# Kernel tuning notes

Measured on AMD Instinct MI355X. Metric: run time of the kernel, lower is better.

The kernel has to match this reference:

```python
import jax, jax.numpy as jnp
import numpy as np

BN_EPS = 1e-5

def _conv1x1(x, w, b):
    # x: [B,C,H,W], w: [O,C], b: [O] -> [B,O,H,W]
    return jnp.einsum('bchw,oc->bohw', x, w) + b[None, :, None, None]

def setup_inputs() -> dict:
    key = jax.random.key(0)
    ks = jax.random.split(key, 9)
    B, C, H, W = 8, 256, 64, 64
    I = C // 2
    s_in = 1.0 / np.sqrt(C)
    s_out = 1.0 / np.sqrt(I)
    return {
        'x':       jax.random.normal(ks[0], (B, C, H, W), dtype=jnp.float32),
        'g_w':     jax.random.uniform(ks[1], (I, C), jnp.float32, -s_in, s_in),
        'g_b':     jax.random.uniform(ks[2], (I,),  jnp.float32, -s_in, s_in),
        'theta_w': jax.random.uniform(ks[3], (I, C), jnp.float32, -s_in, s_in),
        'theta_b': jax.random.uniform(ks[4], (I,),  jnp.float32, -s_in, s_in),
        'phi_w':   jax.random.uniform(ks[5], (I, C), jnp.float32, -s_in, s_in),
        'phi_b':   jax.random.uniform(ks[6], (I,),  jnp.float32, -s_in, s_in),
        'w_w':     jax.random.uniform(ks[7], (C, I), jnp.float32, -s_out, s_out),
        'w_b':     jax.random.uniform(ks[8], (C,),  jnp.float32, -s_out, s_out),
        'gamma':   jnp.ones((C,), dtype=jnp.float32),   # BN weight init constant 1
        'beta':    jnp.zeros((C,), dtype=jnp.float32),  # BN bias init constant 0
    }

def reference(x, g_w, g_b, theta_w, theta_b, phi_w, phi_b, w_w, w_b, gamma, beta):
    B, C, H, W = x.shape
    I = g_w.shape[0]
    N = H * W
    g_x     = _conv1x1(x, g_w, g_b).reshape(B, I, N)          # [B,I,N]
    theta_x = _conv1x1(x, theta_w, theta_b).reshape(B, I, N)  # [B,I,N]
    phi_x   = _conv1x1(x, phi_w, phi_b).reshape(B, I, N)      # [B,I,N]
    # f = theta^T @ phi : [B,N,N]
    f = jnp.einsum('bin,bim->bnm', theta_x, phi_x)
    a = jax.nn.softmax(f, axis=-1)
    # y = a @ g^T : [B,N,I] -> [B,I,H,W]
    y = jnp.einsum('bnm,bim->bin', a, g_x).reshape(B, I, H, W)
    wy = _conv1x1(y, w_w, w_b)                                # [B,C,H,W]
    # BatchNorm2d (training mode: batch statistics over B,H,W per channel)
    mean = jnp.mean(wy, axis=(0, 2, 3), keepdims=True)
    var = jnp.var(wy, axis=(0, 2, 3), keepdims=True)
    wy_bn = (wy - mean) * jax.lax.rsqrt(var + BN_EPS)
    wy_bn = wy_bn * gamma[None, :, None, None] + beta[None, :, None, None]
    return wy_bn + x
```

## Files before the change

kernel.cpp:

```cpp
#include <hip/hip_runtime.h>

#define B_ 8
#define C_ 256
#define I_ 128
#define N_ 4096
#define BN_ (B_ * N_)
#define LOG2E 1.4426950408889634f

typedef __attribute__((ext_vector_type(8))) short bf16x8;
typedef __attribute__((ext_vector_type(4))) float f32x4;
typedef __attribute__((ext_vector_type(4))) int i32x4;

static __device__ __forceinline__ short f2bf(float f) {
    unsigned u = __float_as_uint(f);
    unsigned r = u + 0x7fffu + ((u >> 16) & 1u);
    return (short)(r >> 16);
}
static __device__ __forceinline__ float bf2f(short s) {
    return __uint_as_float(((unsigned)(unsigned short)s) << 16);
}
static __device__ __forceinline__ unsigned cvt_pk_bf16(float lo, float hi) {
    unsigned r;
    asm("v_cvt_pk_bf16_f32 %0, %1, %2" : "=v"(r) : "v"(lo), "v"(hi));
    return r;
}

__global__ void k_prep(const float* g_w, const float* theta_w, const float* phi_w,
                       const float* g_b, const float* theta_b, const float* phi_b,
                       const float* w_w, short* wcat, short* wwb, float* bcat) {
    int i = blockIdx.x * 256 + threadIdx.x;
    if (i < 384 * 256) {
        int j = i >> 8, c = i & 255;
        float v = (j < 128) ? theta_w[j * 256 + c] * LOG2E
                : (j < 256) ? phi_w[(j - 128) * 256 + c]
                            : g_w[(j - 256) * 256 + c];
        wcat[i] = f2bf(v);
    } else if (i < 384 * 256 + 256 * 128) {
        int k = i - 384 * 256;
        wwb[k] = f2bf(w_w[k]);
    } else if (i < 384 * 256 + 256 * 128 + 384) {
        int j = i - (384 * 256 + 256 * 128);
        bcat[j] = (j < 128) ? theta_b[j] * LOG2E
                : (j < 256) ? phi_b[j - 128] : g_b[j - 256];
    }
}

__global__ __launch_bounds__(256) void k_proj(const float* __restrict__ x,
                                              const short* __restrict__ wcat,
                                              const float* __restrict__ bcat,
                                              short* __restrict__ tp,
                                              short* __restrict__ gmat) {
    int b = blockIdx.y;
    int n0 = blockIdx.x * 64;
    int tid = threadIdx.x;
    int wave = tid >> 6, lane = tid & 63, s = lane & 15, q = lane >> 4;
    __shared__ short xs[64][264];

#pragma unroll
    for (int it = 0; it < 16; ++it) {
        int cr = (tid >> 4) + it * 16;
        int nc = tid & 15;
        const float4 v = *(const float4*)&x[((size_t)b * C_ + cr) * N_ + n0 + nc * 4];
        xs[nc * 4 + 0][cr] = f2bf(v.x);
        xs[nc * 4 + 1][cr] = f2bf(v.y);
        xs[nc * 4 + 2][cr] = f2bf(v.z);
        xs[nc * 4 + 3][cr] = f2bf(v.w);
    }
    __syncthreads();

    f32x4 acc[4][6];
#pragma unroll
    for (int rt = 0; rt < 4; ++rt)
#pragma unroll
        for (int jt = 0; jt < 6; ++jt) acc[rt][jt] = (f32x4){0.f, 0.f, 0.f, 0.f};

#pragma unroll
    for (int kb = 0; kb < 8; ++kb) {
        bf16x8 af[4], bfv[6];
#pragma unroll
        for (int rt = 0; rt < 4; ++rt)
            af[rt] = *(const bf16x8*)&xs[rt * 16 + s][kb * 32 + q * 8];
#pragma unroll
        for (int jt = 0; jt < 6; ++jt)
            bfv[jt] = *(const bf16x8*)&wcat[(wave * 96 + jt * 16 + s) * 256 + kb * 32 + q * 8];
#pragma unroll
        for (int rt = 0; rt < 4; ++rt)
#pragma unroll
            for (int jt = 0; jt < 6; ++jt)
                acc[rt][jt] = __builtin_amdgcn_mfma_f32_16x16x32_bf16(af[rt], bfv[jt], acc[rt][jt], 0, 0, 0);
    }

#pragma unroll
    for (int rt = 0; rt < 4; ++rt)
#pragma unroll
        for (int jt = 0; jt < 6; ++jt) {
            int j = wave * 96 + jt * 16 + s;
            float bias = bcat[j];
#pragma unroll
            for (int r = 0; r < 4; ++r) {
                int n = n0 + rt * 16 + 4 * q + r;
                float v = acc[rt][jt][r] + bias;
                if (j < 256)
                    tp[((size_t)b * N_ + n) * 256 + j] = f2bf(v);
                else
                    gmat[((size_t)b * I_ + (j - 256)) * N_ + n] = f2bf(v);
            }
        }
}

__global__ __launch_bounds__(512, 2) void k_attn_wy(const short* __restrict__ tp,
                                                    const short* __restrict__ gmat,
                                                    const short* __restrict__ wwb,
                                                    const float* __restrict__ w_b,
                                                    short* __restrict__ wyh) {
    int id = blockIdx.x;
    int b = id & 7;
    int qt = id >> 3;
    int n0 = qt * 128;
    int tid = threadIdx.x;
    int wave = tid >> 6, lane = tid & 63, s = lane & 15, q = lane >> 4;
    int kg = wave >> 2, qg = wave & 3;

    __shared__ __align__(16) short SH[65536];
    __shared__ float l_lds[2][128];
    char* base = (char*)SH;

    const int swz = (s & 7) << 4;
    int kA[4];
#pragma unroll
    for (int kb = 0; kb < 4; ++kb) kA[kb] = s * 256 + ((kb * 64 + q * 16) ^ swz);
    int vA[2];
#pragma unroll
    for (int kb2 = 0; kb2 < 2; ++kb2) vA[kb2] = s * 256 + ((kb2 * 64 + q * 16) ^ swz);
    int krow = tid >> 4, kch = tid & 15;
    int stW = krow * 256 + ((kch * 16) ^ ((krow & 7) << 4));

    i32x4 onesw = (i32x4){0x3F803F80, 0x3F803F80, 0x3F803F80, 0x3F803F80};
    bf16x8 vone = __builtin_bit_cast(bf16x8, onesw);

    bf16x8 qf[2][4];
#pragma unroll
    for (int fr = 0; fr < 2; ++fr) {
        const short* qb = tp + ((size_t)b * N_ + n0 + qg * 32 + fr * 16 + s) * 256;
#pragma unroll
        for (int kb = 0; kb < 4; ++kb) qf[fr][kb] = *(const bf16x8*)(qb + kb * 32 + q * 8);
    }

    f32x4 ot[2][8];
#pragma unroll
    for (int fr = 0; fr < 2; ++fr)
#pragma unroll
        for (int t = 0; t < 8; ++t) ot[fr][t] = (f32x4){0.f, 0.f, 0.f, 0.f};
    f32x4 lacc[2] = {(f32x4){0.f, 0.f, 0.f, 0.f}, (f32x4){0.f, 0.f, 0.f, 0.f}};

    bf16x8 pk[4], pv[4];
#pragma unroll
    for (int it = 0; it < 4; ++it) {
        pk[it] = *(const bf16x8*)&tp[((size_t)b * N_ + krow + it * 32) * 256 + 128 + kch * 8];
        pv[it] = *(const bf16x8*)&gmat[((size_t)b * I_ + krow + it * 32) * N_ + kch * 8];
    }
#pragma unroll
    for (int it = 0; it < 4; ++it) {
        *(bf16x8*)(base + stW + it * 8192) = pk[it];
        *(bf16x8*)(base + 32768 + stW + it * 8192) = pv[it];
    }
    __syncthreads();

    const int hK = kg * 16384, hV = kg * 128;

    for (int i = 0; i < 32; ++i) {
        char* KtB = base + (i & 1) * 65536;
        char* VtB = KtB + 32768;
        if (i < 31) {
            int m = (i + 1) * 128;
#pragma unroll
            for (int it = 0; it < 4; ++it) {
                pk[it] = *(const bf16x8*)&tp[((size_t)b * N_ + m + krow + it * 32) * 256 + 128 + kch * 8];
                pv[it] = *(const bf16x8*)&gmat[((size_t)b * I_ + krow + it * 32) * N_ + m + kch * 8];
            }
        }

        f32x4 sa[2][4];
#pragma unroll
        for (int fr = 0; fr < 2; ++fr)
#pragma unroll
            for (int tc = 0; tc < 4; ++tc) sa[fr][tc] = (f32x4){0.f, 0.f, 0.f, 0.f};
        __builtin_amdgcn_s_setprio(1);
#pragma unroll
        for (int tc = 0; tc < 4; ++tc) {
            bf16x8 bfv[4];
#pragma unroll
            for (int kb = 0; kb < 4; ++kb)
                bfv[kb] = *(const bf16x8*)(KtB + hK + kA[kb] + tc * 4096);
#pragma unroll
            for (int fr = 0; fr < 2; ++fr)
#pragma unroll
                for (int kb = 0; kb < 4; ++kb)
                    sa[fr][tc] = __builtin_amdgcn_mfma_f32_16x16x32_bf16(bfv[kb], qf[fr][kb], sa[fr][tc], 0, 0, 0);
        }
        __builtin_amdgcn_s_setprio(0);

        unsigned W[2][4][2];
#pragma unroll
        for (int fr = 0; fr < 2; ++fr) {
#pragma unroll
            for (int tc = 0; tc < 4; ++tc)
#pragma unroll
                for (int r = 0; r < 4; ++r) sa[fr][tc][r] = exp2f(sa[fr][tc][r]);
#pragma unroll
            for (int tc = 0; tc < 4; ++tc) {
                W[fr][tc][0] = cvt_pk_bf16(sa[fr][tc][0], sa[fr][tc][1]);
                W[fr][tc][1] = cvt_pk_bf16(sa[fr][tc][2], sa[fr][tc][3]);
            }
        }

#pragma unroll
        for (int kb2 = 0; kb2 < 2; ++kb2) {
            bf16x8 pa[2];
#pragma unroll
            for (int fr = 0; fr < 2; ++fr) {
                unsigned rA = W[fr][2 * kb2 + 0][0];
                unsigned rB = W[fr][2 * kb2 + 0][1];
                unsigned rC = W[fr][2 * kb2 + 1][0];
                unsigned rD = W[fr][2 * kb2 + 1][1];
                asm("v_permlane32_swap_b32 %0, %1" : "+v"(rA), "+v"(rC));
                asm("v_permlane32_swap_b32 %0, %1" : "+v"(rB), "+v"(rD));
                asm("v_permlane16_swap_b32 %0, %1" : "+v"(rA), "+v"(rC));
                asm("v_permlane16_swap_b32 %0, %1" : "+v"(rB), "+v"(rD));
                i32x4 wv = (i32x4){(int)rA, (int)rB, (int)rC, (int)rD};
                pa[fr] = __builtin_bit_cast(bf16x8, wv);
            }
            __builtin_amdgcn_s_setprio(1);
            lacc[0] = __builtin_amdgcn_mfma_f32_16x16x32_bf16(pa[0], vone, lacc[0], 0, 0, 0);
            lacc[1] = __builtin_amdgcn_mfma_f32_16x16x32_bf16(pa[1], vone, lacc[1], 0, 0, 0);
#pragma unroll
            for (int t = 0; t < 8; ++t) {
                bf16x8 vb = *(const bf16x8*)(VtB + hV + vA[kb2] + t * 4096);
                ot[0][t] = __builtin_amdgcn_mfma_f32_16x16x32_bf16(pa[0], vb, ot[0][t], 0, 0, 0);
                ot[1][t] = __builtin_amdgcn_mfma_f32_16x16x32_bf16(pa[1], vb, ot[1][t], 0, 0, 0);
            }
            __builtin_amdgcn_s_setprio(0);
        }

        if (i < 31) {
            char* KtN = base + ((i & 1) ^ 1) * 65536;
#pragma unroll
            for (int it = 0; it < 4; ++it) {
                *(bf16x8*)(KtN + stW + it * 8192) = pk[it];
                *(bf16x8*)(KtN + 32768 + stW + it * 8192) = pv[it];
            }
        }
        __syncthreads();
    }

    if (s == 0) {
#pragma unroll
        for (int fr = 0; fr < 2; ++fr)
#pragma unroll
            for (int r = 0; r < 4; ++r)
                l_lds[kg][qg * 32 + fr * 16 + 4 * q + r] = lacc[fr][r];
    }
    if (kg == 1) {
#pragma unroll
        for (int fr = 0; fr < 2; ++fr)
#pragma unroll
            for (int t = 0; t < 8; ++t)
#pragma unroll
                for (int r = 0; r < 4; ++r) {
                    int row = qg * 32 + fr * 16 + 4 * q + r;
                    int colb = (t * 16 + s) * 4;
                    *(float*)(base + row * 512 + (colb ^ ((row & 7) << 4))) = ot[fr][t][r];
                }
    }
    __syncthreads();
    if (kg == 0) {
#pragma unroll
        for (int fr = 0; fr < 2; ++fr)
#pragma unroll
            for (int t = 0; t < 8; ++t)
#pragma unroll
                for (int r = 0; r < 4; ++r) {
                    int row = qg * 32 + fr * 16 + 4 * q + r;
                    int colb = (t * 16 + s) * 4;
                    float p = *(const float*)(base + row * 512 + (colb ^ ((row & 7) << 4)));
                    float v = ot[fr][t][r] + p;
                    int byt = 65536 + row * 256 + (((t * 16 + s) * 2) ^ ((row & 7) << 4));
                    *(short*)(base + byt) = f2bf(v);
                }
    }
    __syncthreads();

    f32x4 acc[2][8];
#pragma unroll
    for (int ct = 0; ct < 2; ++ct)
#pragma unroll
        for (int jt = 0; jt < 8; ++jt) acc[ct][jt] = (f32x4){0.f, 0.f, 0.f, 0.f};
#pragma unroll
    for (int kb = 0; kb < 4; ++kb) {
        bf16x8 af[2];
#pragma unroll
        for (int ct = 0; ct < 2; ++ct)
            af[ct] = *(const bf16x8*)&wwb[(wave * 32 + ct * 16 + s) * 128 + kb * 32 + q * 8];
#pragma unroll
        for (int jt = 0; jt < 8; ++jt) {
            bf16x8 yb = *(const bf16x8*)(base + 65536 + kA[kb] + jt * 4096);
#pragma unroll
            for (int ct = 0; ct < 2; ++ct)
                acc[ct][jt] = __builtin_amdgcn_mfma_f32_16x16x32_bf16(af[ct], yb, acc[ct][jt], 0, 0, 0);
        }
    }
    float linv[8];
#pragma unroll
    for (int jt = 0; jt < 8; ++jt)
        linv[jt] = 1.0f / (l_lds[0][jt * 16 + s] + l_lds[1][jt * 16 + s]);
#pragma unroll
    for (int ct = 0; ct < 2; ++ct)
#pragma unroll
        for (int r = 0; r < 4; ++r) {
            int c = wave * 32 + ct * 16 + 4 * q + r;
            float bias = w_b[c];
#pragma unroll
            for (int jt = 0; jt < 8; ++jt)
                wyh[((size_t)b * C_ + c) * N_ + n0 + jt * 16 + s] =
                    f2bf(acc[ct][jt][r] * linv[jt] + bias);
        }
}

__global__ __launch_bounds__(256) void k_stats(const short* __restrict__ wyh,
                                               const float* __restrict__ gamma,
                                               const float* __restrict__ beta,
                                               float* __restrict__ scale,
                                               float* __restrict__ shift) {
    int c = blockIdx.x;
    int tid = threadIdx.x;
    float s1 = 0.f, s2 = 0.f;
    for (int b = 0; b < B_; ++b) {
        const short* p = wyh + ((size_t)b * C_ + c) * N_;
        for (int idx = tid * 8; idx < N_; idx += 2048) {
            bf16x8 v = *(const bf16x8*)&p[idx];
#pragma unroll
            for (int j = 0; j < 8; ++j) {
                float f = bf2f(v[j]);
                s1 += f;
                s2 += f * f;
            }
        }
    }
#pragma unroll
    for (int off = 1; off < 64; off <<= 1) {
        s1 += __shfl_xor(s1, off);
        s2 += __shfl_xor(s2, off);
    }
    __shared__ float r1[4], r2[4];
    if ((tid & 63) == 0) { r1[tid >> 6] = s1; r2[tid >> 6] = s2; }
    __syncthreads();
    if (tid == 0) {
        float t1 = r1[0] + r1[1] + r1[2] + r1[3];
        float t2 = r2[0] + r2[1] + r2[2] + r2[3];
        const float inv = 1.0f / 32768.0f;
        float mean = t1 * inv;
        float var = t2 * inv - mean * mean;
        float sc = gamma[c] * rsqrtf(var + 1e-5f);
        scale[c] = sc;
        shift[c] = beta[c] - mean * sc;
    }
}

__global__ __launch_bounds__(256) void k_out(const short* __restrict__ wyh,
                                             const float* __restrict__ x,
                                             const float* __restrict__ scale,
                                             const float* __restrict__ shift,
                                             float* __restrict__ out) {
    int gid = blockIdx.x * 256 + threadIdx.x;
    size_t base = (size_t)gid * 8;
    int c = (int)((base >> 12) & 255);
    float sc = scale[c], sh = shift[c];
    bf16x8 w = *(const bf16x8*)&wyh[base];
    float4 x0 = *(const float4*)&x[base];
    float4 x1 = *(const float4*)&x[base + 4];
    float4 o0, o1;
    o0.x = bf2f(w[0]) * sc + sh + x0.x;
    o0.y = bf2f(w[1]) * sc + sh + x0.y;
    o0.z = bf2f(w[2]) * sc + sh + x0.z;
    o0.w = bf2f(w[3]) * sc + sh + x0.w;
    o1.x = bf2f(w[4]) * sc + sh + x1.x;
    o1.y = bf2f(w[5]) * sc + sh + x1.y;
    o1.z = bf2f(w[6]) * sc + sh + x1.z;
    o1.w = bf2f(w[7]) * sc + sh + x1.w;
    *(float4*)&out[base] = o0;
    *(float4*)&out[base + 4] = o1;
}

extern "C" void kernel_launch(void* const* d_in, const int* in_sizes, int n_in,
                              void* d_out, int out_size, void* d_ws, size_t ws_size,
                              hipStream_t stream) {
    const float* x       = (const float*)d_in[0];
    const float* g_w     = (const float*)d_in[1];
    const float* g_b     = (const float*)d_in[2];
    const float* theta_w = (const float*)d_in[3];
    const float* theta_b = (const float*)d_in[4];
    const float* phi_w   = (const float*)d_in[5];
    const float* phi_b   = (const float*)d_in[6];
    const float* w_w     = (const float*)d_in[7];
    const float* w_b     = (const float*)d_in[8];
    const float* gamma   = (const float*)d_in[9];
    const float* beta    = (const float*)d_in[10];

    char* ws = (char*)d_ws;
    size_t off = 0;
    auto alloc = [&](size_t bytes) {
        void* p = ws + off;
        off += (bytes + 255) & ~(size_t)255;
        return p;
    };
    short*  wcat  = (short*)alloc((size_t)384 * 256 * 2);
    short*  wwb   = (short*)alloc((size_t)256 * 128 * 2);
    float*  bcat  = (float*)alloc((size_t)384 * 4);
    float*  scale = (float*)alloc(256 * 4);
    float*  shift = (float*)alloc(256 * 4);
    short*  tp    = (short*)alloc((size_t)BN_ * 256 * 2);
    short*  gmat  = (short*)alloc((size_t)B_ * I_ * N_ * 2);
    short*  wyh   = (short*)alloc((size_t)BN_ * C_ * 2);

    k_prep<<<514, 256, 0, stream>>>(g_w, theta_w, phi_w, g_b, theta_b, phi_b, w_w,
                                    wcat, wwb, bcat);
    k_proj<<<dim3(64, 8), 256, 0, stream>>>(x, wcat, bcat, tp, gmat);
    k_attn_wy<<<256, 512, 0, stream>>>(tp, gmat, wwb, w_b, wyh);
    k_stats<<<256, 256, 0, stream>>>(wyh, gamma, beta, scale, shift);
    k_out<<<4096, 256, 0, stream>>>(wyh, x, scale, shift, (float*)d_out);
}
```

Baseline: 227.2 us.

## Use async global-to-LDS loads in attention and fuse BN stats via atomics

The K/V tile prefetch in the attention kernel now uses global_load_lds direct-to-LDS copies instead of staging through registers and writing LDS after compute. This frees registers and removes explicit LDS stores. Separately, the BN statistics kernel is removed: the attention epilogue accumulates per-channel sum and sum of squares with atomics, and k_out computes scale/shift inline. This saves a kernel launch and a full read of wyh, but atomics make the reduction order nondeterministic. The async copy has no explicit vmcnt wait beyond __syncthreads, so completion may not be guaranteed before the next iteration reads the buffer.

```diff
diff --git a/kernel.cpp b/kernel.cpp
--- a/kernel.cpp
+++ b/kernel.cpp
@@ -24,10 +24,16 @@
     asm("v_cvt_pk_bf16_f32 %0, %1, %2" : "=v"(r) : "v"(lo), "v"(hi));
     return r;
 }
+static __device__ __forceinline__ void async_copy16(const void* g, void* l) {
+    __builtin_amdgcn_global_load_lds(
+        (const __attribute__((address_space(1))) void*)g,
+        (__attribute__((address_space(3))) void*)l, 16, 0, 0);
+}
 
 __global__ void k_prep(const float* g_w, const float* theta_w, const float* phi_w,
                        const float* g_b, const float* theta_b, const float* phi_b,
-                       const float* w_w, short* wcat, short* wwb, float* bcat) {
+                       const float* w_w, short* wcat, short* wwb, float* bcat,
+                       float* bnsum) {
     int i = blockIdx.x * 256 + threadIdx.x;
     if (i < 384 * 256) {
         int j = i >> 8, c = i & 255;
@@ -42,6 +48,8 @@
         int j = i - (384 * 256 + 256 * 128);
         bcat[j] = (j < 128) ? theta_b[j] * LOG2E
                 : (j < 256) ? phi_b[j - 128] : g_b[j - 256];
+    } else if (i < 384 * 256 + 256 * 128 + 384 + 512) {
+        bnsum[i - (384 * 256 + 256 * 128 + 384)] = 0.f;
     }
 }
 
@@ -112,7 +120,8 @@
                                                     const short* __restrict__ gmat,
                                                     const short* __restrict__ wwb,
                                                     const float* __restrict__ w_b,
-                                                    short* __restrict__ wyh) {
+                                                    short* __restrict__ wyh,
+                                                    float* __restrict__ bnsum) {
     int id = blockIdx.x;
     int b = id & 7;
     int qt = id >> 3;
@@ -132,8 +141,12 @@
     int vA[2];
 #pragma unroll
     for (int kb2 = 0; kb2 < 2; ++kb2) vA[kb2] = s * 256 + ((kb2 * 64 + q * 16) ^ swz);
-    int krow = tid >> 4, kch = tid & 15;
-    int stW = krow * 256 + ((kch * 16) ^ ((krow & 7) << 4));
+
+    int rl = lane >> 4;
+    int colS = ((lane & 15) * 16) ^ ((((wave & 1) << 2) | rl) << 4);
+    const char* gK = (const char*)tp + ((size_t)b * N_ + wave * 4 + rl) * 512 + 256 + colS;
+    const char* gV = (const char*)gmat + ((size_t)b * I_ + wave * 4 + rl) * 8192 + colS;
+    const int ldsSt = wave * 1024;
 
     i32x4 onesw = (i32x4){0x3F803F80, 0x3F803F80, 0x3F803F80, 0x3F803F80};
     bf16x8 vone = __builtin_bit_cast(bf16x8, onesw);
@@ -153,16 +166,10 @@
         for (int t = 0; t < 8; ++t) ot[fr][t] = (f32x4){0.f, 0.f, 0.f, 0.f};
     f32x4 lacc[2] = {(f32x4){0.f, 0.f, 0.f, 0.f}, (f32x4){0.f, 0.f, 0.f, 0.f}};
 
-    bf16x8 pk[4], pv[4];
 #pragma unroll
     for (int it = 0; it < 4; ++it) {
-        pk[it] = *(const bf16x8*)&tp[((size_t)b * N_ + krow + it * 32) * 256 + 128 + kch * 8];
-        pv[it] = *(const bf16x8*)&gmat[((size_t)b * I_ + krow + it * 32) * N_ + kch * 8];
-    }
-#pragma unroll
-    for (int it = 0; it < 4; ++it) {
-        *(bf16x8*)(base + stW + it * 8192) = pk[it];
-        *(bf16x8*)(base + 32768 + stW + it * 8192) = pv[it];
+        async_copy16(gK + it * 16384, base + ldsSt + it * 8192);
+        async_copy16(gV + it * 262144, base + 32768 + ldsSt + it * 8192);
     }
     __syncthreads();
 
@@ -172,11 +179,12 @@
         char* KtB = base + (i & 1) * 65536;
         char* VtB = KtB + 32768;
         if (i < 31) {
-            int m = (i + 1) * 128;
+            char* Kd = base + (((i & 1) ^ 1) * 65536) + ldsSt;
+            size_t m = (size_t)(i + 1) * 128;
 #pragma unroll
             for (int it = 0; it < 4; ++it) {
-                pk[it] = *(const bf16x8*)&tp[((size_t)b * N_ + m + krow + it * 32) * 256 + 128 + kch * 8];
-                pv[it] = *(const bf16x8*)&gmat[((size_t)b * I_ + krow + it * 32) * N_ + m + kch * 8];
+                async_copy16(gK + m * 512 + it * 16384, Kd + it * 8192);
+                async_copy16(gV + m * 2 + it * 262144, Kd + 32768 + it * 8192);
             }
         }
 
@@ -241,15 +249,6 @@
             }
             __builtin_amdgcn_s_setprio(0);
         }
-
-        if (i < 31) {
-            char* KtN = base + ((i & 1) ^ 1) * 65536;
-#pragma unroll
-            for (int it = 0; it < 4; ++it) {
-                *(bf16x8*)(KtN + stW + it * 8192) = pk[it];
-                *(bf16x8*)(KtN + 32768 + stW + it * 8192) = pv[it];
-            }
-        }
         __syncthreads();
     }
 
@@ -319,62 +318,42 @@
         for (int r = 0; r < 4; ++r) {
             int c = wave * 32 + ct * 16 + 4 * q + r;
             float bias = w_b[c];
-#pragma unroll
-            for (int jt = 0; jt < 8; ++jt)
-                wyh[((size_t)b * C_ + c) * N_ + n0 + jt * 16 + s] =
-                    f2bf(acc[ct][jt][r] * linv[jt] + bias);
-        }
-}
-
-__global__ __launch_bounds__(256) void k_stats(const short* __restrict__ wyh,
-                                               const float* __restrict__ gamma,
-                                               const float* __restrict__ beta,
-                                               float* __restrict__ scale,
-                                               float* __restrict__ shift) {
-    int c = blockIdx.x;
-    int tid = threadIdx.x;
-    float s1 = 0.f, s2 = 0.f;
-    for (int b = 0; b < B_; ++b) {
-        const short* p = wyh + ((size_t)b * C_ + c) * N_;
-        for (int idx = tid * 8; idx < N_; idx += 2048) {
-            bf16x8 v = *(const bf16x8*)&p[idx];
-#pragma unroll
-            for (int j = 0; j < 8; ++j) {
-                float f = bf2f(v[j]);
-                s1 += f;
-                s2 += f * f;
-            }
-        }
-    }
-#pragma unroll
-    for (int off = 1; off < 64; off <<= 1) {
-        s1 += __shfl_xor(s1, off);
-        s2 += __shfl_xor(s2, off);
-    }
-    __shared__ float r1[4], r2[4];
-    if ((tid & 63) == 0) { r1[tid >> 6] = s1; r2[tid >> 6] = s2; }
-    __syncthreads();
-    if (tid == 0) {
-        float t1 = r1[0] + r1[1] + r1[2] + r1[3];
-        float t2 = r2[0] + r2[1] + r2[2] + r2[3];
-        const float inv = 1.0f / 32768.0f;
-        float mean = t1 * inv;
-        float var = t2 * inv - mean * mean;
-        float sc = gamma[c] * rsqrtf(var + 1e-5f);
-        scale[c] = sc;
-        shift[c] = beta[c] - mean * sc;
-    }
+            float s1 = 0.f, s2 = 0.f;
+#pragma unroll
+            for (int jt = 0; jt < 8; ++jt) {
+                float v = acc[ct][jt][r] * linv[jt] + bias;
+                short w = f2bf(v);
+                wyh[((size_t)b * C_ + c) * N_ + n0 + jt * 16 + s] = w;
+                float vr = bf2f(w);
+                s1 += vr;
+                s2 += vr * vr;
+            }
+#pragma unroll
+            for (int off = 1; off < 16; off <<= 1) {
+                s1 += __shfl_xor(s1, off);
+                s2 += __shfl_xor(s2, off);
+            }
+            if (s == 0) {
+                atomicAdd(&bnsum[c], s1);
+                atomicAdd(&bnsum[256 + c], s2);
+            }
+        }
 }
 
 __global__ __launch_bounds__(256) void k_out(const short* __restrict__ wyh,
                                              const float* __restrict__ x,
-                                             const float* __restrict__ scale,
-                                             const float* __restrict__ shift,
+                                             const float* __restrict__ bnsum,
+                                             const float* __restrict__ gamma,
+                                             const float* __restrict__ beta,
                                              float* __restrict__ out) {
     int gid = blockIdx.x * 256 + threadIdx.x;
     size_t base = (size_t)gid * 8;
     int c = (int)((base >> 12) & 255);
-    float sc = scale[c], sh = shift[c];
+    const float inv = 1.0f / 32768.0f;
+    float mean = bnsum[c] * inv;
+    float var = bnsum[256 + c] * inv - mean * mean;
+    float sc = gamma[c] * rsqrtf(var + 1e-5f);
+    float sh = beta[c] - mean * sc;
     bf16x8 w = *(const bf16x8*)&wyh[base];
     float4 x0 = *(const float4*)&x[base];
     float4 x1 = *(const float4*)&x[base + 4];
@@ -416,16 +395,14 @@
     short*  wcat  = (short*)alloc((size_t)384 * 256 * 2);
     short*  wwb   = (short*)alloc((size_t)256 * 128 * 2);
     float*  bcat  = (float*)alloc((size_t)384 * 4);
-    float*  scale = (float*)alloc(256 * 4);
-    float*  shift = (float*)alloc(256 * 4);
+    float*  bnsum = (float*)alloc(512 * 4);
     short*  tp    = (short*)alloc((size_t)BN_ * 256 * 2);
     short*  gmat  = (short*)alloc((size_t)B_ * I_ * N_ * 2);
     short*  wyh   = (short*)alloc((size_t)BN_ * C_ * 2);
 
-    k_prep<<<514, 256, 0, stream>>>(g_w, theta_w, phi_w, g_b, theta_b, phi_b, w_w,
-                                    wcat, wwb, bcat);
+    k_prep<<<516, 256, 0, stream>>>(g_w, theta_w, phi_w, g_b, theta_b, phi_b, w_w,
+                                    wcat, wwb, bcat, bnsum);
     k_proj<<<dim3(64, 8), 256, 0, stream>>>(x, wcat, bcat, tp, gmat);
-    k_attn_wy<<<256, 512, 0, stream>>>(tp, gmat, wwb, w_b, wyh);
-    k_stats<<<256, 256, 0, stream>>>(wyh, gamma, beta, scale, shift);
-    k_out<<<4096, 256, 0, stream>>>(wyh, x, scale, shift, (float*)d_out);
-}
+    k_attn_wy<<<256, 512, 0, stream>>>(tp, gmat, wwb, w_b, wyh, bnsum);
+    k_out<<<4096, 256, 0, stream>>>(wyh, x, bnsum, gamma, beta, (float*)d_out);
+}
```

New measurement: 252.6 us. 11.2% more time.
